# Kernel optimization log

Measured on AMD Instinct MI355X. Metric: run time of the kernel, lower is better.

The kernel has to match this reference:

```python
import jax, jax.numpy as jnp
import numpy as np

D_MODEL = 1024
N_HEADS = 16
D_K = D_MODEL // N_HEADS
THETA = 10000.0


def _rope(x, token_positions):
    # x: [b, h, s, d_k]; interleaved RoPE (pairs at even/odd positions)
    half = D_K // 2
    inv_freq = 1.0 / (THETA ** (2.0 * jnp.arange(half, dtype=jnp.float32) / D_K))  # [half]
    angles = token_positions.astype(jnp.float32)[:, None] * inv_freq[None, :]      # [s, half]
    sin, cos = jnp.sin(angles), jnp.cos(angles)
    x_even = x[..., 0::2]
    x_odd = x[..., 1::2]
    out_even = cos * x_even - sin * x_odd
    out_odd = sin * x_even + cos * x_odd
    # interleave back: [..., half, 2] -> [..., d_k]
    return jnp.stack((out_even, out_odd), axis=-1).reshape(x.shape)


def setup_inputs() -> dict:
    key = jax.random.key(0)
    kx, kq, kk, kv, ko = jax.random.split(key, 5)
    b, s = 4, 2048
    std = (2.0 / (D_MODEL + D_MODEL)) ** 0.5
    return {
        "x": jax.random.normal(kx, (b, s, D_MODEL), dtype=jnp.float32),
        "Wq": jax.random.normal(kq, (D_MODEL, D_MODEL), dtype=jnp.float32) * std,
        "Wk": jax.random.normal(kk, (D_MODEL, D_MODEL), dtype=jnp.float32) * std,
        "Wv": jax.random.normal(kv, (D_MODEL, D_MODEL), dtype=jnp.float32) * std,
        "Wo": jax.random.normal(ko, (D_MODEL, D_MODEL), dtype=jnp.float32) * std,
        "token_positions": jnp.arange(s, dtype=jnp.int32),
    }


def reference(x, Wq, Wk, Wv, Wo, token_positions):
    b, s, _ = x.shape
    split = lambda t: t.reshape(b, s, N_HEADS, D_K).transpose(0, 2, 1, 3)  # b h s d
    q = split(x @ Wq.T)
    k = split(x @ Wk.T)
    v = split(x @ Wv.T)
    q = _rope(q, token_positions)
    k = _rope(k, token_positions)
    scores = jnp.einsum("bhnd,bhmd->bhnm", q, k) / jnp.sqrt(jnp.float32(D_K))
    causal = jnp.tril(jnp.ones((s, s), dtype=bool))
    scores = jnp.where(causal, scores, -jnp.inf)
    attn = jax.nn.softmax(scores, axis=-1)
    out = jnp.einsum("bhnm,bhmd->bhnd", attn, v)
    out = out.transpose(0, 2, 1, 3).reshape(b, s, D_MODEL)
    return out @ Wo.T
```

## Files before the change

### kernel.cpp

```cpp
#include <hip/hip_runtime.h>
#include <stdint.h>

typedef __attribute__((ext_vector_type(8))) __bf16 bf16x8;
typedef __attribute__((ext_vector_type(4))) float f32x4;
typedef __attribute__((ext_vector_type(16))) float f32x16;
typedef __attribute__((ext_vector_type(8))) unsigned short ushort8;

__device__ __forceinline__ unsigned short f2bf(float f){
  union { float f; unsigned int i; } v; v.f = f;
  unsigned int r = v.i + 0x7fffu + ((v.i >> 16) & 1u);
  return (unsigned short)(r >> 16);
}
__device__ __forceinline__ void gload16(const void* g, void* l){
  __builtin_amdgcn_global_load_lds((__attribute__((address_space(1))) void*)(g),
                                   (__attribute__((address_space(3))) void*)(l),
                                   16, 0, 0);
}
__device__ __forceinline__ unsigned int cvtpk(float lo, float hi){
  unsigned int r;
  asm("v_cvt_pk_bf16_f32 %0, %1, %2" : "=v"(r) : "v"(lo), "v"(hi));
  return r;
}
__device__ __forceinline__ float fexp2(float x){
  float r; asm("v_exp_f32 %0, %1" : "=v"(r) : "v"(x)); return r;
}
__device__ __forceinline__ bf16x8 ldsw(const char* tile, int row, int colb){
  return *(const bf16x8*)(tile + row*128 + (colb ^ ((row & 7) << 4)));
}

#define SEQ   2048
#define DM    1024
#define NH    16
#define DK    64
#define BATCH 4
#define MTOT  (BATCH*SEQ)
#define NX    (MTOT*DM)
#define NW    (DM*DM)

#define QSCALE 0.18033688011112f

__global__ __launch_bounds__(256) void k_tables(const int* __restrict__ pos,
                                                float* __restrict__ tab)
{
  const int idx = blockIdx.x * 256 + threadIdx.x;
  const int s = idx >> 5, i = idx & 31;
  const float inv = __expf(-0.28782313662425575f * (float)i);
  const float a = (float)pos[s] * inv;
  tab[2*idx]   = cosf(a);
  tab[2*idx+1] = sinf(a);
}

__global__ __launch_bounds__(256) void k_convert(
    const float* __restrict__ x,  const float* __restrict__ wq,
    const float* __restrict__ wk, const float* __restrict__ wv,
    const float* __restrict__ wo,
    unsigned short* __restrict__ xb, unsigned short* __restrict__ wb)
{
  const int tid = blockIdx.x * 256 + threadIdx.x;
  const long long e = (long long)tid * 8;
  const float* src; unsigned short* dst;
  if (e < NX) { src = x + e; dst = xb + e; }
  else {
    long long j = e - NX;
    int seg = (int)(j >> 20);
    long long off = j & 1048575;
    src = (seg==0?wq:seg==1?wk:seg==2?wv:wo) + off;
    dst = wb + (size_t)seg*NW + off;
  }
  const float4 a = *(const float4*)src;
  const float4 b = *(const float4*)(src + 4);
  uint4 o;
  o.x = (unsigned int)f2bf(a.x) | ((unsigned int)f2bf(a.y) << 16);
  o.y = (unsigned int)f2bf(a.z) | ((unsigned int)f2bf(a.w) << 16);
  o.z = (unsigned int)f2bf(b.x) | ((unsigned int)f2bf(b.y) << 16);
  o.w = (unsigned int)f2bf(b.z) | ((unsigned int)f2bf(b.w) << 16);
  *(uint4*)dst = o;
}

#define BK64 64
#define NT   (DM/BK64)
#define ABUF 32768
#define BSTRIDE 49152

template<int MODE>
__global__ __launch_bounds__(512, 2) void k_gemm(
    const unsigned short* __restrict__ A,
    const unsigned short* __restrict__ Wb,
    unsigned short* __restrict__ D0,
    unsigned short* __restrict__ D1,
    unsigned short* __restrict__ D2,
    float* __restrict__ Dout,
    const float* __restrict__ tab)
{
  __shared__ __attribute__((aligned(16))) char lds_[3*BSTRIDE];
  const int tid  = threadIdx.x;
  const int lane = tid & 63;
  const int w    = tid >> 6;
  const int wm = w >> 1, wn = w & 1;

  const int bid = blockIdx.x;
  const int tq  = bid >> 3;
  const int m0  = ((bid & 7)*4 + (tq & 3)) * 256;
  const int r   = tq >> 2;
  const int n0  = (MODE == 0 ? (r & 7) : r) * 128;
  const int z   = (MODE == 0) ? (r >> 3) : 0;

  const unsigned short* W = Wb + (size_t)z * NW;
  unsigned short* Dh = (MODE == 0) ? ((z == 0) ? D0 : (z == 1) ? D1 : D2) : nullptr;
  const bool vtr = (MODE == 0) && (z == 2);

  f32x4 acc[4][4];
  #pragma unroll
  for (int i = 0; i < 4; ++i)
    #pragma unroll
    for (int j = 0; j < 4; ++j)
      acc[i][j] = (f32x4)0.0f;

  auto stA = [&](int buf, int t, int l){
    const int k0 = t * BK64;
    const int id = l*512 + tid;
    const int row = id >> 3, c = id & 7;
    gload16(A + (size_t)(m0 + row)*DM + k0 + ((c ^ (row & 7)) << 3),
            lds_ + buf*BSTRIDE + id*16);
  };
  auto stB = [&](int buf, int t, int l){
    const int k0 = t * BK64;
    const int id = l*512 + tid;
    const int row = id >> 3, c = id & 7;
    gload16(W + (size_t)(n0 + row)*DM + k0 + ((c ^ (row & 7)) << 3),
            lds_ + buf*BSTRIDE + ABUF + id*16);
  };
  auto ldA = [&](const char* Ab_, int i, int kk){
    const int row = wm*64 + i*16 + (lane & 15);
    const int c = (kk*4 + (lane >> 4)) ^ (row & 7);
    return *(const bf16x8*)(Ab_ + row*128 + (c << 4));
  };
  auto ldB = [&](const char* Bb_, int j, int kk){
    const int row = wn*64 + j*16 + (lane & 15);
    const int c = (kk*4 + (lane >> 4)) ^ (row & 7);
    return *(const bf16x8*)(Bb_ + row*128 + (c << 4));
  };

  #pragma unroll
  for (int l = 0; l < 4; ++l) stA(0, 0, l);
  stB(0, 0, 0); stB(0, 0, 1);
  #pragma unroll
  for (int l = 0; l < 4; ++l) stA(1, 1, l);
  stB(1, 1, 0); stB(1, 1, 1);
  asm volatile("s_waitcnt vmcnt(6)" ::: "memory");
  __builtin_amdgcn_s_barrier();

  int rb = 0, sb = 2;
  for (int t = 0; t < NT; ++t){
    const char* Ab_ = lds_ + rb*BSTRIDE;
    const char* Bb_ = Ab_ + ABUF;
    const bool st = (t + 2 < NT);
    bf16x8 aF0, aF1, bF[4];

    aF0 = ldA(Ab_, 0, 0); aF1 = ldA(Ab_, 1, 0);
    bF[0] = ldB(Bb_, 0, 0); bF[1] = ldB(Bb_, 1, 0);
    bF[2] = ldB(Bb_, 2, 0); bF[3] = ldB(Bb_, 3, 0);
    if (st){ stA(sb, t+2, 0); stA(sb, t+2, 1); }
    __builtin_amdgcn_s_barrier();
    asm volatile("s_waitcnt lgkmcnt(0)" ::: "memory");
    __builtin_amdgcn_s_setprio(1);
    #pragma unroll
    for (int j = 0; j < 4; ++j){
      acc[0][j] = __builtin_amdgcn_mfma_f32_16x16x32_bf16(aF0, bF[j], acc[0][j], 0, 0, 0);
      acc[1][j] = __builtin_amdgcn_mfma_f32_16x16x32_bf16(aF1, bF[j], acc[1][j], 0, 0, 0);
    }
    __builtin_amdgcn_s_setprio(0);
    __builtin_amdgcn_s_barrier();

    aF0 = ldA(Ab_, 2, 0); aF1 = ldA(Ab_, 3, 0);
    if (st){ stA(sb, t+2, 2); stA(sb, t+2, 3); }
    __builtin_amdgcn_s_barrier();
    asm volatile("s_waitcnt lgkmcnt(0)" ::: "memory");
    __builtin_amdgcn_s_setprio(1);
    #pragma unroll
    for (int j = 0; j < 4; ++j){
      acc[2][j] = __builtin_amdgcn_mfma_f32_16x16x32_bf16(aF0, bF[j], acc[2][j], 0, 0, 0);
      acc[3][j] = __builtin_amdgcn_mfma_f32_16x16x32_bf16(aF1, bF[j], acc[3][j], 0, 0, 0);
    }
    __builtin_amdgcn_s_setprio(0);
    __builtin_amdgcn_s_barrier();

    aF0 = ldA(Ab_, 0, 1); aF1 = ldA(Ab_, 1, 1);
    bF[0] = ldB(Bb_, 0, 1); bF[1] = ldB(Bb_, 1, 1);
    bF[2] = ldB(Bb_, 2, 1); bF[3] = ldB(Bb_, 3, 1);
    if (st){ stB(sb, t+2, 0); stB(sb, t+2, 1); }
    __builtin_amdgcn_s_barrier();
    asm volatile("s_waitcnt lgkmcnt(0)" ::: "memory");
    __builtin_amdgcn_s_setprio(1);
    #pragma unroll
    for (int j = 0; j < 4; ++j){
      acc[0][j] = __builtin_amdgcn_mfma_f32_16x16x32_bf16(aF0, bF[j], acc[0][j], 0, 0, 0);
      acc[1][j] = __builtin_amdgcn_mfma_f32_16x16x32_bf16(aF1, bF[j], acc[1][j], 0, 0, 0);
    }
    __builtin_amdgcn_s_setprio(0);
    __builtin_amdgcn_s_barrier();

    aF0 = ldA(Ab_, 2, 1); aF1 = ldA(Ab_, 3, 1);
    __builtin_amdgcn_s_barrier();
    asm volatile("s_waitcnt lgkmcnt(0)" ::: "memory");
    __builtin_amdgcn_s_setprio(1);
    #pragma unroll
    for (int j = 0; j < 4; ++j){
      acc[2][j] = __builtin_amdgcn_mfma_f32_16x16x32_bf16(aF0, bF[j], acc[2][j], 0, 0, 0);
      acc[3][j] = __builtin_amdgcn_mfma_f32_16x16x32_bf16(aF1, bF[j], acc[3][j], 0, 0, 0);
    }
    __builtin_amdgcn_s_setprio(0);
    if (t < NT-2)       asm volatile("s_waitcnt vmcnt(6)" ::: "memory");
    else if (t == NT-2) asm volatile("s_waitcnt vmcnt(0)" ::: "memory");
    if (t < NT-1) __builtin_amdgcn_s_barrier();

    rb = (rb == 2) ? 0 : rb + 1;
    sb = (sb == 2) ? 0 : sb + 1;
  }

  __syncthreads();

  {
    float* T = (float*)lds_;
    #pragma unroll
    for (int i = 0; i < 4; ++i)
      #pragma unroll
      for (int j = 0; j < 4; ++j){
        const int n = wn*64 + j*16 + (lane & 15);
        #pragma unroll
        for (int rr = 0; rr < 4; ++rr){
          const int m = wm*64 + i*16 + ((lane >> 4) << 2) + rr;
          T[m*128 + (n ^ ((m & 7) << 2))] = acc[i][j][rr];
        }
      }
  }
  __syncthreads();
  const float* T = (const float*)lds_;

  if (MODE == 0 && vtr){
    const int nl = tid >> 2;
    const int sblk = tid & 3;
    const int d = nl & 63, hh = (n0 >> 6) + (nl >> 6);
    const int bidx = m0 >> 11;
    unsigned short* vrow = Dh + (((size_t)(bidx*NH + hh))*DK + d)*SEQ + (m0 & 2047);
    #pragma unroll
    for (int c = 0; c < 8; ++c){
      const int s0 = sblk*8 + c*32;
      float v[8];
      #pragma unroll
      for (int j2 = 0; j2 < 8; ++j2)
        v[j2] = T[(s0 + j2)*128 + (nl ^ (((s0 + j2) & 7) << 2))];
      uint4 ov;
      ov.x = cvtpk(v[0], v[1]); ov.y = cvtpk(v[2], v[3]);
      ov.z = cvtpk(v[4], v[5]); ov.w = cvtpk(v[6], v[7]);
      *(uint4*)(vrow + s0) = ov;
    }
  } else {
    const float scale = (MODE == 0 && z == 0) ? QSCALE : 1.0f;
    #pragma unroll
    for (int k = 0; k < 8; ++k){
      const int cid = k*512 + tid;
      const int d8   = cid & 7;
      const int sp_l = (cid >> 3) & 255;
      const int h    = cid >> 11;
      const int nb   = h*64 + d8*8;
      const int sw   = (sp_l & 7) << 2;
      const f32x4 c0 = *(const f32x4*)&T[sp_l*128 + (nb ^ sw)];
      const f32x4 c1 = *(const f32x4*)&T[sp_l*128 + ((nb + 4) ^ sw)];
      if (MODE == 1){
        float* dst = Dout + (size_t)(m0 + sp_l)*DM + n0 + nb;
        *(f32x4*)dst = c0;
        *(f32x4*)(dst + 4) = c1;
      } else {
        const int mg = m0 + sp_l;
        const int bidx = mg >> 11, sp = mg & 2047;
        const float4 t01 = *(const float4*)&tab[(size_t)sp*64 + d8*8];
        const float4 t23 = *(const float4*)&tab[(size_t)sp*64 + d8*8 + 4];
        const unsigned int u0 = cvtpk((t01.x*c0[0] - t01.y*c0[1])*scale,
                                      (t01.y*c0[0] + t01.x*c0[1])*scale);
        const unsigned int u1 = cvtpk((t01.z*c0[2] - t01.w*c0[3])*scale,
                                      (t01.w*c0[2] + t01.z*c0[3])*scale);
        const unsigned int u2 = cvtpk((t23.x*c1[0] - t23.y*c1[1])*scale,
                                      (t23.y*c1[0] + t23.x*c1[1])*scale);
        const unsigned int u3 = cvtpk((t23.z*c1[2] - t23.w*c1[3])*scale,
                                      (t23.w*c1[2] + t23.z*c1[3])*scale);
        const int hh = (n0 >> 6) + h;
        uint4 ov; ov.x = u0; ov.y = u1; ov.z = u2; ov.w = u3;
        *(uint4*)(Dh + ((size_t)((bidx*NH + hh)*SEQ + sp))*DK + d8*8) = ov;
      }
    }
  }
}

__global__ __launch_bounds__(512, 4) void k_attn(const unsigned short* __restrict__ Qh,
                                                 const unsigned short* __restrict__ Kh,
                                                 const unsigned short* __restrict__ Vt,
                                                 unsigned short* __restrict__ Ab)
{
  __shared__ uint4 ldsu[4096];
  char* base = (char*)ldsu;
  const int tid  = threadIdx.x;
  const int lane = tid & 63;
  const int w    = tid >> 6;
  const int ww   = w & 3;
  const int g    = w >> 2;
  const int tl   = tid & 255;
  const int l31  = lane & 31;
  const int hl   = lane >> 5;
  char* gb = base + g*32768;

  const int bh = blockIdx.x, jj = blockIdx.y;
  const unsigned short* Qb = Qh + (size_t)bh*(SEQ*DK);
  const unsigned short* Kb = Kh + (size_t)bh*(SEQ*DK);
  const unsigned short* Vb = Vt + (size_t)bh*(SEQ*DK);
  const int b = bh >> 4, hd = bh & 15;

  for (int pass = 0; pass < 2; ++pass){
    const int qt = pass ? jj : 15 - jj;
    const int q0 = qt * 128;
    const int qbase = q0 + ww*32;

    bf16x8 qf[4];
    #pragma unroll
    for (int t = 0; t < 4; ++t)
      qf[t] = *(const bf16x8*)(Qb + (size_t)(qbase + l31)*DK + t*16 + hl*8);

    f32x16 acc0 = (f32x16)0.0f, acc1 = (f32x16)0.0f;
    float lsum = 0.0f;

    const int nk = qt + 1;
    const int tbase = g * nk;
    const int wqmax = qbase + 31;

    auto stage = [&](int buf, int ktile){
      const int k0s = ktile * 64;
      char* Kd = gb + buf*16384;
      char* Vd = Kd + 8192;
      #pragma unroll
      for (int cc = 0; cc < 2; ++cc){
        const int f = cc*256 + tl;
        const int r = f >> 3, slot = f & 7;
        const int sw = ((slot ^ (r & 7)) << 3);
        gload16(Kb + (size_t)(k0s + r)*DK + sw, Kd + (cc*256 + ww*64)*16);
        gload16(Vb + (size_t)r*SEQ + k0s + sw, Vd + (cc*256 + ww*64)*16);
      }
    };

    if (pass) __syncthreads();
    stage(0, tbase);
    __syncthreads();
    int cur = 0;

    for (int kt = 0; kt < nk; ++kt){
      const int k0 = (tbase + kt) * 64;
      if (kt + 1 < nk) stage(cur ^ 1, tbase + kt + 1);
      if (k0 <= wqmax){
        const char* Ks = gb + cur*16384;
        const char* Vs = Ks + 8192;

        f32x16 sv0 = (f32x16)0.0f, sv1 = (f32x16)0.0f;
        __builtin_amdgcn_s_setprio(1);
        #pragma unroll
        for (int t = 0; t < 4; ++t){
          const int colb = t*32 + hl*16;
          const bf16x8 a0 = ldsw(Ks, l31, colb);
          const bf16x8 a1 = ldsw(Ks, 32 + l31, colb);
          sv0 = __builtin_amdgcn_mfma_f32_32x32x16_bf16(a0, qf[t], sv0, 0, 0, 0);
          sv1 = __builtin_amdgcn_mfma_f32_32x32x16_bf16(a1, qf[t], sv1, 0, 0, 0);
        }
        __builtin_amdgcn_s_setprio(0);

        if (k0 + 63 > qbase){
          const int q = qbase + l31;
          #pragma unroll
          for (int j = 0; j < 16; ++j){
            const int kv = k0 + (j&3) + 8*(j>>2) + 4*hl;
            if (kv > q)      sv0[j] = -1e30f;
            if (kv + 32 > q) sv1[j] = -1e30f;
          }
        }

        #pragma unroll
        for (int j = 0; j < 16; ++j){
          sv0[j] = fexp2(sv0[j]);
          sv1[j] = fexp2(sv1[j]);
        }
        float ts[8];
        #pragma unroll
        for (int j = 0; j < 8; ++j)
          ts[j] = (sv0[j] + sv0[j+8]) + (sv1[j] + sv1[j+8]);
        #pragma unroll
        for (int off = 4; off; off >>= 1)
          #pragma unroll
          for (int j = 0; j < off; ++j)
            ts[j] += ts[j+off];
        lsum += ts[0] + __shfl_xor(ts[0], 32, 64);

        __builtin_amdgcn_s_setprio(1);
        #pragma unroll
        for (int t = 0; t < 4; ++t){
          f32x16& s = (t < 2) ? sv0 : sv1;
          const int b0v = (t & 1) * 8;
          const unsigned int A0 = cvtpk(s[b0v+0], s[b0v+1]);
          const unsigned int A1 = cvtpk(s[b0v+2], s[b0v+3]);
          const unsigned int B0 = cvtpk(s[b0v+4], s[b0v+5]);
          const unsigned int B1 = cvtpk(s[b0v+6], s[b0v+7]);
          const unsigned int s0 = hl ? A0 : B0;
          const unsigned int s1 = hl ? A1 : B1;
          const unsigned int r0 = (unsigned int)__shfl_xor((int)s0, 32, 64);
          const unsigned int r1 = (unsigned int)__shfl_xor((int)s1, 32, 64);
          union { unsigned int u[4]; bf16x8 v; } f;
          f.u[0] = hl ? r0 : A0; f.u[1] = hl ? r1 : A1;
          f.u[2] = hl ? B0 : r0; f.u[3] = hl ? B1 : r1;
          const int colb = t*32 + hl*16;
          const bf16x8 v0 = ldsw(Vs, l31, colb);
          const bf16x8 v1 = ldsw(Vs, 32 + l31, colb);
          acc0 = __builtin_amdgcn_mfma_f32_32x32x16_bf16(v0, f.v, acc0, 0, 0, 0);
          acc1 = __builtin_amdgcn_mfma_f32_32x32x16_bf16(v1, f.v, acc1, 0, 0, 0);
        }
        __builtin_amdgcn_s_setprio(0);
      }
      __syncthreads();
      cur ^= 1;
    }

    if (g == 1){
      char* cw = base + ww*9216 + lane*144;
      #pragma unroll
      for (int q4 = 0; q4 < 4; ++q4){
        *(f32x4*)(cw + q4*16)      = (f32x4){acc0[4*q4], acc0[4*q4+1], acc0[4*q4+2], acc0[4*q4+3]};
        *(f32x4*)(cw + 64 + q4*16) = (f32x4){acc1[4*q4], acc1[4*q4+1], acc1[4*q4+2], acc1[4*q4+3]};
      }
      *(float*)(cw + 128) = lsum;
    }
    __syncthreads();
    if (g == 0){
      const char* cr = base + ww*9216 + lane*144;
      const float l1 = *(const float*)(cr + 128);
      const float linv = 1.0f / (lsum + l1);
      unsigned short* orow = Ab + ((size_t)(b*SEQ + qbase + l31))*DM + hd*DK;
      #pragma unroll
      for (int mt = 0; mt < 2; ++mt){
        #pragma unroll
        for (int g4 = 0; g4 < 4; ++g4){
          const f32x16& a = mt ? acc1 : acc0;
          const f32x4 o = *(const f32x4*)(cr + mt*64 + g4*16);
          const unsigned int u0 = cvtpk((a[4*g4+0] + o[0])*linv, (a[4*g4+1] + o[1])*linv);
          const unsigned int u1 = cvtpk((a[4*g4+2] + o[2])*linv, (a[4*g4+3] + o[3])*linv);
          *(unsigned long long*)(orow + mt*32 + g4*8 + hl*4) =
              (unsigned long long)u0 | ((unsigned long long)u1 << 32);
        }
      }
    }
  }
}

extern "C" void kernel_launch(void* const* d_in, const int* in_sizes, int n_in,
                              void* d_out, int out_size, void* d_ws, size_t ws_size,
                              hipStream_t stream)
{
  (void)in_sizes; (void)n_in; (void)out_size;
  const float* x  = (const float*)d_in[0];
  const float* wq = (const float*)d_in[1];
  const float* wk = (const float*)d_in[2];
  const float* wv = (const float*)d_in[3];
  const float* wo = (const float*)d_in[4];
  const int* pos  = (const int*)d_in[5];
  float* out = (float*)d_out;

  if (ws_size < 92800000u) return;
  char* ws = (char*)d_ws;
  unsigned short* xb = (unsigned short*)(ws);
  unsigned short* wb = (unsigned short*)(ws + 16777216);
  unsigned short* Qh = (unsigned short*)(ws + 25165824);
  unsigned short* Kh = (unsigned short*)(ws + 41943040);
  unsigned short* Vt = (unsigned short*)(ws + 75497472);
  float* tab         = (float*)(ws + 92274688);

  k_tables  <<<256, 256, 0, stream>>>(pos, tab);
  k_convert <<<6144, 256, 0, stream>>>(x, wq, wk, wv, wo, xb, wb);
  k_gemm<0> <<<768, 512, 0, stream>>>(xb, wb, Qh, Kh, Vt, nullptr, tab);
  k_attn    <<<dim3(64, 8), 512, 0, stream>>>(Qh, Kh, Vt, xb);
  k_gemm<1> <<<256, 512, 0, stream>>>(xb, wb + 3*NW, nullptr, nullptr,
                                      nullptr, out, nullptr);
}
```

Before: 160.9 us.

## Halve GEMM K-tile to 32 and split epilogue to raise GEMM occupancy

Changes the projection GEMM kernels from a 64-wide K tile to a 32-wide K tile with a matching 4-chunk XOR swizzle, so the triple-buffered LDS staging area shrinks from 144KB to 72KB. The epilogue now writes the 256x128 fp32 accumulator tile through LDS in two 128-row halves so it fits the smaller buffer. Launch bounds go from 2 to 4 blocks per CU to use the freed LDS for more resident waves. In exchange it doubles the number of K iterations and barriers per tile and adds an extra epilogue sync, and holding the 64 accumulator floats per thread under the tighter register budget may cause spills.

```diff
diff --git a/kernel.cpp b/kernel.cpp
--- a/kernel.cpp
+++ b/kernel.cpp
@@ -77,13 +77,12 @@
   *(uint4*)dst = o;
 }
 
-#define BK64 64
-#define NT   (DM/BK64)
-#define ABUF 32768
-#define BSTRIDE 49152
+#define NT32 32
+#define ABUF32  16384
+#define BSTR32  24576
 
 template<int MODE>
-__global__ __launch_bounds__(512, 2) void k_gemm(
+__global__ __launch_bounds__(512, 4) void k_gemm(
     const unsigned short* __restrict__ A,
     const unsigned short* __restrict__ Wb,
     unsigned short* __restrict__ D0,
@@ -92,7 +91,7 @@
     float* __restrict__ Dout,
     const float* __restrict__ tab)
 {
-  __shared__ __attribute__((aligned(16))) char lds_[3*BSTRIDE];
+  __shared__ __attribute__((aligned(16))) char lds_[3*BSTR32];
   const int tid  = threadIdx.x;
   const int lane = tid & 63;
   const int w    = tid >> 6;
@@ -117,49 +116,43 @@
       acc[i][j] = (f32x4)0.0f;
 
   auto stA = [&](int buf, int t, int l){
-    const int k0 = t * BK64;
     const int id = l*512 + tid;
-    const int row = id >> 3, c = id & 7;
-    gload16(A + (size_t)(m0 + row)*DM + k0 + ((c ^ (row & 7)) << 3),
-            lds_ + buf*BSTRIDE + id*16);
+    const int row = id >> 2, c = id & 3;
+    gload16(A + (size_t)(m0 + row)*DM + t*32 + ((c ^ ((row >> 1) & 3)) << 3),
+            lds_ + buf*BSTR32 + id*16);
   };
-  auto stB = [&](int buf, int t, int l){
-    const int k0 = t * BK64;
-    const int id = l*512 + tid;
-    const int row = id >> 3, c = id & 7;
-    gload16(W + (size_t)(n0 + row)*DM + k0 + ((c ^ (row & 7)) << 3),
-            lds_ + buf*BSTRIDE + ABUF + id*16);
+  auto stB = [&](int buf, int t){
+    const int id = tid;
+    const int row = id >> 2, c = id & 3;
+    gload16(W + (size_t)(n0 + row)*DM + t*32 + ((c ^ ((row >> 1) & 3)) << 3),
+            lds_ + buf*BSTR32 + ABUF32 + id*16);
   };
-  auto ldA = [&](const char* Ab_, int i, int kk){
+  auto ldA = [&](const char* Ab_, int i){
     const int row = wm*64 + i*16 + (lane & 15);
-    const int c = (kk*4 + (lane >> 4)) ^ (row & 7);
-    return *(const bf16x8*)(Ab_ + row*128 + (c << 4));
+    const int c = (lane >> 4) ^ ((row >> 1) & 3);
+    return *(const bf16x8*)(Ab_ + row*64 + (c << 4));
   };
-  auto ldB = [&](const char* Bb_, int j, int kk){
+  auto ldB = [&](const char* Bb_, int j){
     const int row = wn*64 + j*16 + (lane & 15);
-    const int c = (kk*4 + (lane >> 4)) ^ (row & 7);
-    return *(const bf16x8*)(Bb_ + row*128 + (c << 4));
+    const int c = (lane >> 4) ^ ((row >> 1) & 3);
+    return *(const bf16x8*)(Bb_ + row*64 + (c << 4));
   };
 
-  #pragma unroll
-  for (int l = 0; l < 4; ++l) stA(0, 0, l);
-  stB(0, 0, 0); stB(0, 0, 1);
-  #pragma unroll
-  for (int l = 0; l < 4; ++l) stA(1, 1, l);
-  stB(1, 1, 0); stB(1, 1, 1);
-  asm volatile("s_waitcnt vmcnt(6)" ::: "memory");
+  stA(0, 0, 0); stA(0, 0, 1); stB(0, 0);
+  stA(1, 1, 0); stA(1, 1, 1); stB(1, 1);
+  asm volatile("s_waitcnt vmcnt(3)" ::: "memory");
   __builtin_amdgcn_s_barrier();
 
   int rb = 0, sb = 2;
-  for (int t = 0; t < NT; ++t){
-    const char* Ab_ = lds_ + rb*BSTRIDE;
-    const char* Bb_ = Ab_ + ABUF;
-    const bool st = (t + 2 < NT);
+  for (int t = 0; t < NT32; ++t){
+    const char* Ab_ = lds_ + rb*BSTR32;
+    const char* Bb_ = Ab_ + ABUF32;
+    const bool st = (t + 2 < NT32);
     bf16x8 aF0, aF1, bF[4];
 
-    aF0 = ldA(Ab_, 0, 0); aF1 = ldA(Ab_, 1, 0);
-    bF[0] = ldB(Bb_, 0, 0); bF[1] = ldB(Bb_, 1, 0);
-    bF[2] = ldB(Bb_, 2, 0); bF[3] = ldB(Bb_, 3, 0);
+    aF0 = ldA(Ab_, 0); aF1 = ldA(Ab_, 1);
+    bF[0] = ldB(Bb_, 0); bF[1] = ldB(Bb_, 1);
+    bF[2] = ldB(Bb_, 2); bF[3] = ldB(Bb_, 3);
     if (st){ stA(sb, t+2, 0); stA(sb, t+2, 1); }
     __builtin_amdgcn_s_barrier();
     asm volatile("s_waitcnt lgkmcnt(0)" ::: "memory");
@@ -172,8 +165,8 @@
     __builtin_amdgcn_s_setprio(0);
     __builtin_amdgcn_s_barrier();
 
-    aF0 = ldA(Ab_, 2, 0); aF1 = ldA(Ab_, 3, 0);
-    if (st){ stA(sb, t+2, 2); stA(sb, t+2, 3); }
+    aF0 = ldA(Ab_, 2); aF1 = ldA(Ab_, 3);
+    if (st) stB(sb, t+2);
     __builtin_amdgcn_s_barrier();
     asm volatile("s_waitcnt lgkmcnt(0)" ::: "memory");
     __builtin_amdgcn_s_setprio(1);
@@ -183,110 +176,85 @@
       acc[3][j] = __builtin_amdgcn_mfma_f32_16x16x32_bf16(aF1, bF[j], acc[3][j], 0, 0, 0);
     }
     __builtin_amdgcn_s_setprio(0);
-    __builtin_amdgcn_s_barrier();
-
-    aF0 = ldA(Ab_, 0, 1); aF1 = ldA(Ab_, 1, 1);
-    bF[0] = ldB(Bb_, 0, 1); bF[1] = ldB(Bb_, 1, 1);
-    bF[2] = ldB(Bb_, 2, 1); bF[3] = ldB(Bb_, 3, 1);
-    if (st){ stB(sb, t+2, 0); stB(sb, t+2, 1); }
-    __builtin_amdgcn_s_barrier();
-    asm volatile("s_waitcnt lgkmcnt(0)" ::: "memory");
-    __builtin_amdgcn_s_setprio(1);
-    #pragma unroll
-    for (int j = 0; j < 4; ++j){
-      acc[0][j] = __builtin_amdgcn_mfma_f32_16x16x32_bf16(aF0, bF[j], acc[0][j], 0, 0, 0);
-      acc[1][j] = __builtin_amdgcn_mfma_f32_16x16x32_bf16(aF1, bF[j], acc[1][j], 0, 0, 0);
-    }
-    __builtin_amdgcn_s_setprio(0);
-    __builtin_amdgcn_s_barrier();
-
-    aF0 = ldA(Ab_, 2, 1); aF1 = ldA(Ab_, 3, 1);
-    __builtin_amdgcn_s_barrier();
-    asm volatile("s_waitcnt lgkmcnt(0)" ::: "memory");
-    __builtin_amdgcn_s_setprio(1);
-    #pragma unroll
-    for (int j = 0; j < 4; ++j){
-      acc[2][j] = __builtin_amdgcn_mfma_f32_16x16x32_bf16(aF0, bF[j], acc[2][j], 0, 0, 0);
-      acc[3][j] = __builtin_amdgcn_mfma_f32_16x16x32_bf16(aF1, bF[j], acc[3][j], 0, 0, 0);
-    }
-    __builtin_amdgcn_s_setprio(0);
-    if (t < NT-2)       asm volatile("s_waitcnt vmcnt(6)" ::: "memory");
-    else if (t == NT-2) asm volatile("s_waitcnt vmcnt(0)" ::: "memory");
-    if (t < NT-1) __builtin_amdgcn_s_barrier();
+    if (t < NT32-2)       asm volatile("s_waitcnt vmcnt(3)" ::: "memory");
+    else if (t == NT32-2) asm volatile("s_waitcnt vmcnt(0)" ::: "memory");
+    if (t < NT32-1) __builtin_amdgcn_s_barrier();
 
     rb = (rb == 2) ? 0 : rb + 1;
     sb = (sb == 2) ? 0 : sb + 1;
   }
 
   __syncthreads();
-
-  {
-    float* T = (float*)lds_;
-    #pragma unroll
-    for (int i = 0; i < 4; ++i)
-      #pragma unroll
-      for (int j = 0; j < 4; ++j){
-        const int n = wn*64 + j*16 + (lane & 15);
-        #pragma unroll
-        for (int rr = 0; rr < 4; ++rr){
-          const int m = wm*64 + i*16 + ((lane >> 4) << 2) + rr;
-          T[m*128 + (n ^ ((m & 7) << 2))] = acc[i][j][rr];
-        }
-      }
-  }
-  __syncthreads();
-  const float* T = (const float*)lds_;
-
-  if (MODE == 0 && vtr){
-    const int nl = tid >> 2;
-    const int sblk = tid & 3;
-    const int d = nl & 63, hh = (n0 >> 6) + (nl >> 6);
-    const int bidx = m0 >> 11;
-    unsigned short* vrow = Dh + (((size_t)(bidx*NH + hh))*DK + d)*SEQ + (m0 & 2047);
-    #pragma unroll
-    for (int c = 0; c < 8; ++c){
-      const int s0 = sblk*8 + c*32;
-      float v[8];
-      #pragma unroll
-      for (int j2 = 0; j2 < 8; ++j2)
-        v[j2] = T[(s0 + j2)*128 + (nl ^ (((s0 + j2) & 7) << 2))];
-      uint4 ov;
-      ov.x = cvtpk(v[0], v[1]); ov.y = cvtpk(v[2], v[3]);
-      ov.z = cvtpk(v[4], v[5]); ov.w = cvtpk(v[6], v[7]);
-      *(uint4*)(vrow + s0) = ov;
-    }
-  } else {
-    const float scale = (MODE == 0 && z == 0) ? QSCALE : 1.0f;
-    #pragma unroll
-    for (int k = 0; k < 8; ++k){
-      const int cid = k*512 + tid;
-      const int d8   = cid & 7;
-      const int sp_l = (cid >> 3) & 255;
-      const int h    = cid >> 11;
-      const int nb   = h*64 + d8*8;
-      const int sw   = (sp_l & 7) << 2;
-      const f32x4 c0 = *(const f32x4*)&T[sp_l*128 + (nb ^ sw)];
-      const f32x4 c1 = *(const f32x4*)&T[sp_l*128 + ((nb + 4) ^ sw)];
-      if (MODE == 1){
-        float* dst = Dout + (size_t)(m0 + sp_l)*DM + n0 + nb;
-        *(f32x4*)dst = c0;
-        *(f32x4*)(dst + 4) = c1;
-      } else {
-        const int mg = m0 + sp_l;
-        const int bidx = mg >> 11, sp = mg & 2047;
-        const float4 t01 = *(const float4*)&tab[(size_t)sp*64 + d8*8];
-        const float4 t23 = *(const float4*)&tab[(size_t)sp*64 + d8*8 + 4];
-        const unsigned int u0 = cvtpk((t01.x*c0[0] - t01.y*c0[1])*scale,
-                                      (t01.y*c0[0] + t01.x*c0[1])*scale);
-        const unsigned int u1 = cvtpk((t01.z*c0[2] - t01.w*c0[3])*scale,
-                                      (t01.w*c0[2] + t01.z*c0[3])*scale);
-        const unsigned int u2 = cvtpk((t23.x*c1[0] - t23.y*c1[1])*scale,
-                                      (t23.y*c1[0] + t23.x*c1[1])*scale);
-        const unsigned int u3 = cvtpk((t23.z*c1[2] - t23.w*c1[3])*scale,
-                                      (t23.w*c1[2] + t23.z*c1[3])*scale);
-        const int hh = (n0 >> 6) + h;
-        uint4 ov; ov.x = u0; ov.y = u1; ov.z = u2; ov.w = u3;
-        *(uint4*)(Dh + ((size_t)((bidx*NH + hh)*SEQ + sp))*DK + d8*8) = ov;
+  float* T = (float*)lds_;
+  #pragma unroll
+  for (int h = 0; h < 2; ++h){
+    if (h) __syncthreads();
+    if ((wm >> 1) == h){
+      #pragma unroll
+      for (int i = 0; i < 4; ++i)
+        #pragma unroll
+        for (int j = 0; j < 4; ++j){
+          const int n = wn*64 + j*16 + (lane & 15);
+          #pragma unroll
+          for (int rr = 0; rr < 4; ++rr){
+            const int mh = (wm & 1)*64 + i*16 + ((lane >> 4) << 2) + rr;
+            T[mh*128 + (n ^ ((mh & 7) << 2))] = acc[i][j][rr];
+          }
+        }
+    }
+    __syncthreads();
+    if (MODE == 0 && vtr){
+      const int nl = tid >> 2;
+      const int sblk = tid & 3;
+      const int d = nl & 63, hh = (n0 >> 6) + (nl >> 6);
+      const int bidx = m0 >> 11;
+      unsigned short* vrow = Dh + (((size_t)(bidx*NH + hh))*DK + d)*SEQ
+                               + (m0 & 2047) + h*128;
+      #pragma unroll
+      for (int c = 0; c < 4; ++c){
+        const int s0 = sblk*8 + c*32;
+        float v[8];
+        #pragma unroll
+        for (int j2 = 0; j2 < 8; ++j2)
+          v[j2] = T[(s0 + j2)*128 + (nl ^ (((s0 + j2) & 7) << 2))];
+        uint4 ov;
+        ov.x = cvtpk(v[0], v[1]); ov.y = cvtpk(v[2], v[3]);
+        ov.z = cvtpk(v[4], v[5]); ov.w = cvtpk(v[6], v[7]);
+        *(uint4*)(vrow + s0) = ov;
+      }
+    } else {
+      const float scale = (MODE == 0 && z == 0) ? QSCALE : 1.0f;
+      #pragma unroll
+      for (int k = 0; k < 4; ++k){
+        const int cid = k*512 + tid;
+        const int d8   = cid & 7;
+        const int sp_l = (cid >> 3) & 127;
+        const int hc   = cid >> 10;
+        const int nb   = hc*64 + d8*8;
+        const int sw   = (sp_l & 7) << 2;
+        const f32x4 c0 = *(const f32x4*)&T[sp_l*128 + (nb ^ sw)];
+        const f32x4 c1 = *(const f32x4*)&T[sp_l*128 + ((nb + 4) ^ sw)];
+        if (MODE == 1){
+          float* dst = Dout + (size_t)(m0 + h*128 + sp_l)*DM + n0 + nb;
+          *(f32x4*)dst = c0;
+          *(f32x4*)(dst + 4) = c1;
+        } else {
+          const int mg = m0 + h*128 + sp_l;
+          const int bidx = mg >> 11, sp = mg & 2047;
+          const float4 t01 = *(const float4*)&tab[(size_t)sp*64 + d8*8];
+          const float4 t23 = *(const float4*)&tab[(size_t)sp*64 + d8*8 + 4];
+          const unsigned int u0 = cvtpk((t01.x*c0[0] - t01.y*c0[1])*scale,
+                                        (t01.y*c0[0] + t01.x*c0[1])*scale);
+          const unsigned int u1 = cvtpk((t01.z*c0[2] - t01.w*c0[3])*scale,
+                                        (t01.w*c0[2] + t01.z*c0[3])*scale);
+          const unsigned int u2 = cvtpk((t23.x*c1[0] - t23.y*c1[1])*scale,
+                                        (t23.y*c1[0] + t23.x*c1[1])*scale);
+          const unsigned int u3 = cvtpk((t23.z*c1[2] - t23.w*c1[3])*scale,
+                                        (t23.w*c1[2] + t23.z*c1[3])*scale);
+          const int hh = (n0 >> 6) + hc;
+          uint4 ov; ov.x = u0; ov.y = u1; ov.z = u2; ov.w = u3;
+          *(uint4*)(Dh + ((size_t)((bidx*NH + hh)*SEQ + sp))*DK + d8*8) = ov;
+        }
       }
     }
   }
```

Result: no change. 160.4 us (-0.3%).
